# Optimization experiments

Measured on AMD Instinct MI355X. Metric: run time of the kernel, lower is better.

Reference implementation:

```python
import jax, jax.numpy as jnp
import numpy as np

HALF_LOG_2PI = 0.5 * float(np.log(2.0 * np.pi))


def setup_inputs() -> dict:
    key = jax.random.key(0)
    k1, k2 = jax.random.split(key)
    N, D = 16384, 2048
    x = jax.random.normal(k1, (N, D), dtype=jnp.float32)
    raw_params = jax.random.normal(k2, (2 * D,), dtype=jnp.float32)
    # chain spanning tree: edges (i, i+1) for i in 0..D-2  -> shape [D-1, 2]
    idx = jnp.arange(D - 1, dtype=jnp.int64)
    edges = jnp.stack([idx, idx + 1], axis=1)
    return {"x": x, "raw_params": raw_params, "edges": edges}


def reference(x, raw_params, edges):
    # x: [N, D] float; raw_params: [2D] float; edges: [E, 2] int
    D = x.shape[1]
    means = jnp.tanh(raw_params[:D]) * 2.0               # [D]
    stds = jax.nn.softplus(raw_params[D:]) + 1e-6         # [D]
    # Each edge (i, j) contributes logN(x_i) + logN(x_j); equivalently each
    # feature k contributes deg(k) * logN(x_k), deg = endpoint multiplicity.
    deg = jnp.zeros((D,), dtype=x.dtype).at[edges.reshape(-1)].add(1.0)  # [D]
    z = (x - means) / stds                                # [N, D]
    logp = -0.5 * z * z - jnp.log(stds) - HALF_LOG_2PI    # [N, D]
    return logp @ deg                                     # [N]
```

## Files before the change

kernel.cpp:

```cpp
#include <hip/hip_runtime.h>
#include <math.h>

#define HALF_LOG_2PI_F 0.9189385332046727f

__global__ void clt_prep_kernel(const float* __restrict__ rp,
                                const int* __restrict__ edges,
                                float* __restrict__ A,
                                float* __restrict__ B,
                                float* __restrict__ csum,
                                int D, int E) {
    extern __shared__ float sdeg[];
    for (int k = threadIdx.x; k < D; k += blockDim.x) sdeg[k] = 0.0f;
    __syncthreads();
    for (int e = threadIdx.x; e < E; e += blockDim.x) {
        int i = edges[2 * e];
        int j = edges[2 * e + 1];
        atomicAdd(&sdeg[i], 1.0f);
        atomicAdd(&sdeg[j], 1.0f);
    }
    __syncthreads();

    float local_c = 0.0f;
    for (int k = threadIdx.x; k < D; k += blockDim.x) {
        float m = tanhf(rp[k]) * 2.0f;
        float sx = rp[D + k];
        float s = fmaxf(sx, 0.0f) + log1pf(expf(-fabsf(sx))) + 1e-6f;
        float inv_s2 = 1.0f / (s * s);
        float deg = sdeg[k];
        A[k] = deg * (-0.5f * inv_s2);
        B[k] = deg * (m * inv_s2);
        local_c += deg * (-0.5f * m * m * inv_s2 - logf(s) - HALF_LOG_2PI_F);
    }

    __shared__ float wsum[16];
    for (int off = 32; off > 0; off >>= 1)
        local_c += __shfl_down(local_c, off, 64);
    int wid = threadIdx.x >> 6;
    int lane = threadIdx.x & 63;
    if (lane == 0) wsum[wid] = local_c;
    __syncthreads();
    if (threadIdx.x == 0) {
        float t = 0.0f;
        int nw = (blockDim.x + 63) >> 6;
        for (int w = 0; w < nw; ++w) t += wsum[w];
        *csum = t;
    }
}

__global__ __launch_bounds__(256) void clt_row_kernel(
        const float* __restrict__ x,
        const float* __restrict__ A,
        const float* __restrict__ B,
        const float* __restrict__ csum,
        float* __restrict__ out,
        int D) {
    const int row = blockIdx.x;
    const float4* xv = (const float4*)(x + (size_t)row * (size_t)D);
    const float4* Av = (const float4*)A;
    const float4* Bv = (const float4*)B;
    const int nv = D >> 2;

    float acc = 0.0f;
    for (int i = threadIdx.x; i < nv; i += blockDim.x) {
        float4 xq = xv[i];
        float4 aq = Av[i];
        float4 bq = Bv[i];
        acc += xq.x * fmaf(aq.x, xq.x, bq.x);
        acc += xq.y * fmaf(aq.y, xq.y, bq.y);
        acc += xq.z * fmaf(aq.z, xq.z, bq.z);
        acc += xq.w * fmaf(aq.w, xq.w, bq.w);
    }
    for (int k = (nv << 2) + threadIdx.x; k < D; k += blockDim.x) {
        float xs = x[(size_t)row * (size_t)D + k];
        acc += xs * fmaf(A[k], xs, B[k]);
    }

    for (int off = 32; off > 0; off >>= 1)
        acc += __shfl_down(acc, off, 64);
    __shared__ float wsum[4];
    int wid = threadIdx.x >> 6;
    int lane = threadIdx.x & 63;
    if (lane == 0) wsum[wid] = acc;
    __syncthreads();
    if (threadIdx.x == 0) {
        out[row] = wsum[0] + wsum[1] + wsum[2] + wsum[3] + *csum;
    }
}

extern "C" void kernel_launch(void* const* d_in, const int* in_sizes, int n_in,
                              void* d_out, int out_size, void* d_ws, size_t ws_size,
                              hipStream_t stream) {
    const float* x     = (const float*)d_in[0];
    const float* rp    = (const float*)d_in[1];
    const int*   edges = (const int*)d_in[2];
    float* out = (float*)d_out;

    const int D = in_sizes[1] / 2;
    const int E = in_sizes[2] / 2;
    const int N = out_size;

    float* A    = (float*)d_ws;
    float* B    = A + D;
    float* csum = B + D;

    clt_prep_kernel<<<1, 256, D * sizeof(float), stream>>>(rp, edges, A, B, csum, D, E);
    clt_row_kernel<<<N, 256, 0, stream>>>(x, A, B, csum, out, D);
}
```

Baseline: 39.80 us.

## Assign one wavefront per row with register-cached coefficients and persistent grid

Replaces the block-per-row kernel with a templated kernel where each 64-lane wavefront processes whole rows in a grid-stride loop. The per-feature coefficients A and B are loaded into registers once per wave and reused across rows. The cross-wave shared-memory reduction and __syncthreads are replaced by a shuffle-only reduction. The prep kernel also launches with 1024 threads. Holding NI float4 pairs per lane adds register pressure (64 VGPRs for D=2048), which may reduce occupancy for this memory-bound read of x.

```diff
diff --git a/kernel.cpp b/kernel.cpp
--- a/kernel.cpp
+++ b/kernel.cpp
@@ -47,7 +47,47 @@
     }
 }
 
-__global__ __launch_bounds__(256) void clt_row_kernel(
+template <int NI>
+__global__ __launch_bounds__(256) void clt_rows_fast(
+        const float* __restrict__ x,
+        const float* __restrict__ A,
+        const float* __restrict__ B,
+        const float* __restrict__ csum,
+        float* __restrict__ out,
+        int D, int N, int total_waves) {
+    const int lane = threadIdx.x & 63;
+    const int gwave = blockIdx.x * (blockDim.x >> 6) + (threadIdx.x >> 6);
+
+    const float4* Av = (const float4*)A;
+    const float4* Bv = (const float4*)B;
+    float4 a4[NI], b4[NI];
+#pragma unroll
+    for (int i = 0; i < NI; ++i) {
+        a4[i] = Av[i * 64 + lane];
+        b4[i] = Bv[i * 64 + lane];
+    }
+    const float c = *csum;
+
+    for (int r = gwave; r < N; r += total_waves) {
+        const float4* xv = (const float4*)(x + (size_t)r * (size_t)D);
+        float acc0 = 0.0f, acc1 = 0.0f;
+#pragma unroll
+        for (int i = 0; i < NI; ++i) {
+            float4 xq = xv[i * 64 + lane];
+            acc0 += xq.x * fmaf(a4[i].x, xq.x, b4[i].x);
+            acc1 += xq.y * fmaf(a4[i].y, xq.y, b4[i].y);
+            acc0 += xq.z * fmaf(a4[i].z, xq.z, b4[i].z);
+            acc1 += xq.w * fmaf(a4[i].w, xq.w, b4[i].w);
+        }
+        float acc = acc0 + acc1;
+#pragma unroll
+        for (int off = 32; off > 0; off >>= 1)
+            acc += __shfl_down(acc, off, 64);
+        if (lane == 0) out[r] = acc + c;
+    }
+}
+
+__global__ __launch_bounds__(256) void clt_row_generic(
         const float* __restrict__ x,
         const float* __restrict__ A,
         const float* __restrict__ B,
@@ -55,26 +95,11 @@
         float* __restrict__ out,
         int D) {
     const int row = blockIdx.x;
-    const float4* xv = (const float4*)(x + (size_t)row * (size_t)D);
-    const float4* Av = (const float4*)A;
-    const float4* Bv = (const float4*)B;
-    const int nv = D >> 2;
-
     float acc = 0.0f;
-    for (int i = threadIdx.x; i < nv; i += blockDim.x) {
-        float4 xq = xv[i];
-        float4 aq = Av[i];
-        float4 bq = Bv[i];
-        acc += xq.x * fmaf(aq.x, xq.x, bq.x);
-        acc += xq.y * fmaf(aq.y, xq.y, bq.y);
-        acc += xq.z * fmaf(aq.z, xq.z, bq.z);
-        acc += xq.w * fmaf(aq.w, xq.w, bq.w);
-    }
-    for (int k = (nv << 2) + threadIdx.x; k < D; k += blockDim.x) {
+    for (int k = threadIdx.x; k < D; k += blockDim.x) {
         float xs = x[(size_t)row * (size_t)D + k];
         acc += xs * fmaf(A[k], xs, B[k]);
     }
-
     for (int off = 32; off > 0; off >>= 1)
         acc += __shfl_down(acc, off, 64);
     __shared__ float wsum[4];
@@ -82,9 +107,8 @@
     int lane = threadIdx.x & 63;
     if (lane == 0) wsum[wid] = acc;
     __syncthreads();
-    if (threadIdx.x == 0) {
+    if (threadIdx.x == 0)
         out[row] = wsum[0] + wsum[1] + wsum[2] + wsum[3] + *csum;
-    }
 }
 
 extern "C" void kernel_launch(void* const* d_in, const int* in_sizes, int n_in,
@@ -103,6 +127,22 @@
     float* B    = A + D;
     float* csum = B + D;
 
-    clt_prep_kernel<<<1, 256, D * sizeof(float), stream>>>(rp, edges, A, B, csum, D, E);
-    clt_row_kernel<<<N, 256, 0, stream>>>(x, A, B, csum, out, D);
+    clt_prep_kernel<<<1, 1024, D * sizeof(float), stream>>>(rp, edges, A, B, csum, D, E);
+
+    const int NI = D / 256;
+    if (D % 256 == 0 && (NI == 2 || NI == 4 || NI == 8 || NI == 16)) {
+        int waves = (N + 3) / 4;
+        int blocks = (waves + 3) / 4;
+        if (blocks < 64) blocks = 64;
+        if (blocks > 4096) blocks = 4096;
+        int total_waves = blocks * 4;
+        switch (NI) {
+            case 2:  clt_rows_fast<2><<<blocks, 256, 0, stream>>>(x, A, B, csum, out, D, N, total_waves); break;
+            case 4:  clt_rows_fast<4><<<blocks, 256, 0, stream>>>(x, A, B, csum, out, D, N, total_waves); break;
+            case 8:  clt_rows_fast<8><<<blocks, 256, 0, stream>>>(x, A, B, csum, out, D, N, total_waves); break;
+            default: clt_rows_fast<16><<<blocks, 256, 0, stream>>>(x, A, B, csum, out, D, N, total_waves); break;
+        }
+    } else {
+        clt_row_generic<<<N, 256, 0, stream>>>(x, A, B, csum, out, D);
+    }
 }
```

Measured after the change: 35.60 us. -10.5%, faster.
